# Kernel tuning notes

Hardware: AMD Instinct MI355X
Metric: run time of the kernel (lower is better)

## Reference

```python
import jax, jax.numpy as jnp
import numpy as np

B, K, N, M = 32, 128, 128, 256  # batch, num_classes(==n_dim), n_dim, samples-per-matrix
EPSILON = 0.1
LAMBDA_SOFTMAX = 0.1
LEARNING_RATE = 0.01
BN_EPS = 1e-5


def setup_inputs() -> dict:
    key = jax.random.key(0)
    k1, k2, k3 = jax.random.split(key, 3)
    x = jax.random.normal(k1, (B, N, M), dtype=jnp.float32)
    A = jax.random.normal(k2, (K, N, N), dtype=jnp.float32) * 0.1
    EC_proto = jnp.einsum('kij,klj->kil', A, A)  # per-class PSD prototype covariances (K,N,N)
    EC_count = jax.random.uniform(k3, (K,), dtype=jnp.float32, minval=1.0, maxval=100.0)
    return {"x": x, "EC_proto": EC_proto, "EC_count": EC_count}


def reference(x, EC_proto, EC_count):
    n = x.shape[1]
    dtype = x.dtype
    # BatchNorm1d(num_classes, affine=False, track_running_stats=False): batch stats over (N, L)
    mean = x.mean(axis=(0, 2), keepdims=True)
    var = x.var(axis=(0, 2), keepdims=True)  # biased variance, as torch uses for normalization
    x = (x - mean) / jnp.sqrt(var + BN_EPS)

    eye = jnp.eye(n, dtype=dtype)
    total = EC_count.sum()
    has_counts = total > 1e-6

    # E branch: global expansion operator
    e_alpha = jnp.where(has_counts, n / (EPSILON * EPSILON * total), jnp.zeros((), dtype))
    e = e_alpha * jnp.linalg.inv(e_alpha * EC_proto.sum(0) + eye)  # (N,N)
    e_x_z = jnp.einsum('ij,bjm->bim', e, x)  # (B,N,M)

    # C branch: per-class compression operators
    bool_depth = (EC_count != 0).astype(dtype)  # (K,)
    count_fix = EC_count + (1.0 - bool_depth)
    c_alpha = (n / (count_fix * EPSILON * EPSILON) * bool_depth)[:, None, None]  # (K,1,1)
    c = c_alpha * jnp.linalg.inv(c_alpha * EC_proto + eye[None])  # (K,N,N)
    c_x_z = jnp.einsum('kij,bjm->bkim', c, x)  # (B,K,N,M)

    # Frobenius norm per (b,k), rescaled to sum to 10 over classes
    norm = jnp.sqrt((c_x_z * c_x_z).sum(axis=(2, 3)))  # (B,K)
    norm = 10.0 * norm / norm.sum(axis=1, keepdims=True)

    pi = jax.nn.softmax(-LAMBDA_SOFTMAX * norm, axis=1) * bool_depth  # (B,K)
    gama = jnp.where(has_counts, EC_count / total, jnp.zeros_like(EC_count))  # (K,)

    z_d = e_x_z - jnp.einsum('k,bkim,bk->bim', gama, c_x_z, pi)  # (B,N,M)
    return x + LEARNING_RATE * z_d
```

## Files before the change

### kernel.cpp

```cpp
#include <hip/hip_runtime.h>
#include <math.h>

#define Bb 32
#define Kk 128
#define Nn 128
#define Mm 256
#define EPS2 0.01f
#define LAMBDA_S 0.1f
#define LR 0.01f
#define BN_EPS_C 1e-5f

#define SWZ(c) (((c) & 14) | (((c) & 1) << 4) | (((c) >> 4) & 1))

__device__ __forceinline__ float readlane_f(float v, int lane) {
  return __int_as_float(__builtin_amdgcn_readlane(__float_as_int(v), lane));
}

__global__ void kA_bn_psum(const float* __restrict__ x, const float* __restrict__ P,
                           float* __restrict__ xn, float* __restrict__ Psum) {
  int t = threadIdx.x;
  if (blockIdx.x < 128) {
    int n = blockIdx.x;
    float v[32];
    float s = 0.f, s2 = 0.f;
    #pragma unroll
    for (int b = 0; b < Bb; ++b) {
      v[b] = x[(size_t)b * (Nn * Mm) + n * Mm + t];
      s += v[b];
      s2 += v[b] * v[b];
    }
    #pragma unroll
    for (int o = 32; o > 0; o >>= 1) {
      s += __shfl_down(s, o, 64);
      s2 += __shfl_down(s2, o, 64);
    }
    __shared__ float rs[4], rs2[4];
    if ((t & 63) == 0) { rs[t >> 6] = s; rs2[t >> 6] = s2; }
    __syncthreads();
    float S = rs[0] + rs[1] + rs[2] + rs[3];
    float S2 = rs2[0] + rs2[1] + rs2[2] + rs2[3];
    float mean = S * (1.0f / (Bb * Mm));
    float var = S2 * (1.0f / (Bb * Mm)) - mean * mean;
    float rstd = 1.0f / sqrtf(var + BN_EPS_C);
    #pragma unroll
    for (int b = 0; b < Bb; ++b)
      xn[(size_t)b * (Nn * Mm) + n * Mm + t] = (v[b] - mean) * rstd;
  } else {
    int e = (blockIdx.x - 128) * 256 + t;
    float s = 0.f;
    #pragma unroll 8
    for (int k = 0; k < Kk; ++k) s += P[(size_t)k * 16384 + e];
    Psum[e] = s;
  }
}

__global__ __launch_bounds__(512, 1) void k3S(
    const float* __restrict__ P, const float* __restrict__ Psum,
    const float* __restrict__ cnt, float* __restrict__ C,
    const float* __restrict__ xn, float* __restrict__ S) {
  __shared__ __align__(16) float LB[8448];
  int bx = blockIdx.x;
  int t = threadIdx.x;

  if (bx < 129) {
    float* Mt = LB;
    float* Rb = LB + 2112;
    float* redc = LB + 4160;
    int mat = bx;
    int tx = t & 15;
    int wy = t >> 4;

    float cv = cnt[t & 127];
    float sr = cv;
    #pragma unroll
    for (int o = 32; o > 0; o >>= 1) sr += __shfl_down(sr, o, 64);
    if ((t & 63) == 0) redc[t >> 6] = sr;
    __syncthreads();
    float total = redc[0] + redc[1];
    bool has = total > 1e-6f;
    float av;
    if (mat < 128) {
      float c = cnt[mat];
      float bk = (c != 0.0f) ? 1.0f : 0.0f;
      float cfix = c + (1.0f - bk);
      av = (float)Nn / (cfix * EPS2) * bk;
    } else {
      av = has ? ((float)Nn / (EPS2 * total)) : 0.0f;
    }
    const float* src = (mat < 128) ? (P + (size_t)mat * 16384) : Psum;

    float a[4][8];
    #pragma unroll
    for (int i = 0; i < 4; ++i) {
      int row = wy * 4 + i;
      float4 p0 = *(const float4*)&src[row * 128 + tx * 8];
      float4 p1 = *(const float4*)&src[row * 128 + tx * 8 + 4];
      a[i][0] = av * p0.x; a[i][1] = av * p0.y; a[i][2] = av * p0.z; a[i][3] = av * p0.w;
      a[i][4] = av * p1.x; a[i][5] = av * p1.y; a[i][6] = av * p1.z; a[i][7] = av * p1.w;
      if (tx == (wy >> 1)) a[i][(wy & 1) * 4 + i] += 1.0f;
    }

    for (int kb = 0; kb < 8; ++kb) {
      int k0 = kb * 16;
      if ((wy >> 2) == kb) {
        int d = wy & 3;
        #pragma unroll
        for (int i = 0; i < 4; ++i) {
          *(float4*)&Rb[(d * 4 + i) * 128 + SWZ(2 * tx) * 4] =
              make_float4(a[i][0], a[i][1], a[i][2], a[i][3]);
          *(float4*)&Rb[(d * 4 + i) * 128 + SWZ(2 * tx + 1) * 4] =
              make_float4(a[i][4], a[i][5], a[i][6], a[i][7]);
        }
      }
      if ((tx >> 1) == kb) {
        int dh = tx & 1;
        #pragma unroll
        for (int i = 0; i < 4; ++i)
          #pragma unroll
          for (int j = 0; j < 8; ++j)
            Mt[(dh * 8 + j) * 132 + wy * 4 + i] = a[i][j];
      }
      __syncthreads();

      if (t < 64) {
        int l = t;
        float m[2][16];
        #pragma unroll
        for (int d = 0; d < 2; ++d)
          #pragma unroll
          for (int j = 0; j < 16; ++j)
            m[d][j] = Mt[j * 132 + 2 * l + d];
        #pragma unroll
        for (int q = 0; q < 16; ++q) {
          int lq = (k0 + q) >> 1;
          float pr[16];
          #pragma unroll
          for (int j = 0; j < 16; ++j) pr[j] = readlane_f(m[q & 1][j], lq);
          float piv = pr[q];
          float r0 = __builtin_amdgcn_rcpf(piv);
          float pinv = r0 * (2.0f - piv * r0);
          #pragma unroll
          for (int d = 0; d < 2; ++d) {
            float f = m[d][q];
            bool isp = (2 * l + d == k0 + q);
            float g = isp ? (1.0f - pinv) : f * pinv;
            #pragma unroll
            for (int j = 0; j < 16; ++j) m[d][j] = fmaf(-g, pr[j], m[d][j]);
            m[d][q] = isp ? pinv : -g;
          }
        }
        #pragma unroll
        for (int d = 0; d < 2; ++d)
          #pragma unroll
          for (int j = 0; j < 16; ++j)
            Mt[j * 132 + 2 * l + d] = m[d][j];
      }
      __syncthreads();

      if ((wy >> 2) == kb) {
        #pragma unroll
        for (int i = 0; i < 4; ++i)
          #pragma unroll
          for (int j = 0; j < 8; ++j) a[i][j] = 0.0f;
      }
      #pragma unroll
      for (int q = 0; q < 16; ++q) {
        float4 m0 = *(const float4*)&Mt[q * 132 + wy * 4];
        float4 r0 = *(const float4*)&Rb[q * 128 + SWZ(2 * tx) * 4];
        float4 r1 = *(const float4*)&Rb[q * 128 + SWZ(2 * tx + 1) * 4];
        float mq[4] = {m0.x, m0.y, m0.z, m0.w};
        float rq[8] = {r0.x, r0.y, r0.z, r0.w, r1.x, r1.y, r1.z, r1.w};
        #pragma unroll
        for (int i = 0; i < 4; ++i)
          #pragma unroll
          for (int j = 0; j < 8; ++j)
            a[i][j] = fmaf(mq[i], rq[j], a[i][j]);
      }
      if ((tx >> 1) == kb) {
        int dh = tx & 1;
        #pragma unroll
        for (int j = 0; j < 8; ++j) {
          float4 v0 = *(const float4*)&Mt[(dh * 8 + j) * 132 + wy * 4];
          a[0][j] = v0.x; a[1][j] = v0.y; a[2][j] = v0.z; a[3][j] = v0.w;
        }
      }
      __syncthreads();
    }

    float* dst = C + (size_t)mat * 16384;
    #pragma unroll
    for (int i = 0; i < 4; ++i) {
      int row = wy * 4 + i;
      float4 v0 = make_float4(av * a[i][0], av * a[i][1], av * a[i][2], av * a[i][3]);
      float4 v1 = make_float4(av * a[i][4], av * a[i][5], av * a[i][6], av * a[i][7]);
      *(float4*)&dst[row * 128 + tx * 8] = v0;
      *(float4*)&dst[row * 128 + tx * 8 + 4] = v1;
    }
  } else {
    int bxx = bx - 129;
    int b = bxx >> 1;
    int jbase = (bxx & 1) * 64;
    float* X = LB;
    int tx = t & 15, wy = t >> 4;
    float acc[4][4] = {};
    for (int mc = 0; mc < Mm; mc += 64) {
      __syncthreads();
      #pragma unroll
      for (int c = 0; c < 16; ++c) {
        int e = c * 512 + t;
        int i = e >> 6, mm = e & 63;
        X[i * 65 + mm] = xn[(size_t)b * (Nn * Mm) + i * Mm + mc + mm];
      }
      __syncthreads();
      for (int mm = 0; mm < 64; ++mm) {
        float ai[4], bj[4];
        #pragma unroll
        for (int q = 0; q < 4; ++q) ai[q] = X[(wy * 4 + q) * 65 + mm];
        #pragma unroll
        for (int q = 0; q < 4; ++q) bj[q] = X[(jbase + tx * 4 + q) * 65 + mm];
        #pragma unroll
        for (int qi = 0; qi < 4; ++qi)
          #pragma unroll
          for (int qj = 0; qj < 4; ++qj)
            acc[qi][qj] = fmaf(ai[qi], bj[qj], acc[qi][qj]);
      }
    }
    float* dst = S + (size_t)b * 16384;
    #pragma unroll
    for (int qi = 0; qi < 4; ++qi) {
      float4 v = make_float4(acc[qi][0], acc[qi][1], acc[qi][2], acc[qi][3]);
      *(float4*)&dst[(wy * 4 + qi) * 128 + jbase + tx * 4] = v;
    }
  }
}

__global__ __launch_bounds__(512, 1) void kGN(const float* __restrict__ C,
                                              const float* __restrict__ S,
                                              float* __restrict__ norm2h) {
  __shared__ __align__(16) float LB[128 * 128];
  __shared__ float redb[8][32];
  int k = blockIdx.x >> 1, h = blockIdx.x & 1;
  int t = threadIdx.x;
  const float* src = C + (size_t)k * 16384;
  #pragma unroll
  for (int c = 0; c < 32; ++c) LB[c * 512 + t] = src[c * 512 + t];
  __syncthreads();
  int tx = t & 15, ty = t >> 4;
  int i0 = ty * 4, j0 = h * 64 + tx * 4;
  float acc[4][4] = {};
  for (int l = 0; l < 128; ++l) {
    float ai[4], bj[4];
    *(float4*)&ai[0] = *(const float4*)&LB[l * 128 + i0];
    *(float4*)&bj[0] = *(const float4*)&LB[l * 128 + j0];
    #pragma unroll
    for (int qi = 0; qi < 4; ++qi)
      #pragma unroll
      for (int qj = 0; qj < 4; ++qj)
        acc[qi][qj] = fmaf(ai[qi], bj[qj], acc[qi][qj]);
  }
  float nacc[32];
  #pragma unroll
  for (int b = 0; b < 32; ++b) nacc[b] = 0.0f;
  #pragma unroll
  for (int qi = 0; qi < 4; ++qi) {
    const float* sb = S + (i0 + qi) * 128 + j0;
    #pragma unroll
    for (int b = 0; b < 32; ++b) {
      float4 sv = *(const float4*)&sb[(size_t)b * 16384];
      nacc[b] = fmaf(acc[qi][0], sv.x, nacc[b]);
      nacc[b] = fmaf(acc[qi][1], sv.y, nacc[b]);
      nacc[b] = fmaf(acc[qi][2], sv.z, nacc[b]);
      nacc[b] = fmaf(acc[qi][3], sv.w, nacc[b]);
    }
  }
  #pragma unroll
  for (int b = 0; b < 32; ++b) {
    float v = nacc[b];
    #pragma unroll
    for (int o = 32; o > 0; o >>= 1) v += __shfl_down(v, o, 64);
    nacc[b] = v;
  }
  if ((t & 63) == 0) {
    int w = t >> 6;
    #pragma unroll
    for (int b = 0; b < 32; ++b) redb[w][b] = nacc[b];
  }
  __syncthreads();
  if (t < 32) {
    float s = 0.f;
    #pragma unroll
    for (int w = 0; w < 8; ++w) s += redb[w][t];
    norm2h[(size_t)k * 64 + h * 32 + t] = s;
  }
}

__global__ __launch_bounds__(256, 1) void k8f(const float* __restrict__ C,
                                              const float* __restrict__ E,
                                              const float* __restrict__ norm2h,
                                              const float* __restrict__ cnt,
                                              float* __restrict__ F) {
  int t = threadIdx.x;
  int e = blockIdx.x * 256 + t;
  int b0 = blockIdx.y * 8;
  __shared__ float wTl[128][8];
  __shared__ float redT[2];
  __shared__ float redN[2][8];
  __shared__ float redE[2][8];

  float nb[8];
  float cv = 0.f;
  if (t < 128) {
    int k = t;
    cv = cnt[k];
    #pragma unroll
    for (int j = 0; j < 8; ++j) {
      float n2 = norm2h[(size_t)k * 64 + b0 + j] +
                 norm2h[(size_t)k * 64 + 32 + b0 + j];
      nb[j] = sqrtf(fmaxf(n2, 0.0f));
    }
    float tt = cv;
    float sn[8];
    #pragma unroll
    for (int j = 0; j < 8; ++j) sn[j] = nb[j];
    #pragma unroll
    for (int o = 32; o > 0; o >>= 1) {
      tt += __shfl_down(tt, o, 64);
      #pragma unroll
      for (int j = 0; j < 8; ++j) sn[j] += __shfl_down(sn[j], o, 64);
    }
    if ((t & 63) == 0) {
      redT[t >> 6] = tt;
      #pragma unroll
      for (int j = 0; j < 8; ++j) redN[t >> 6][j] = sn[j];
    }
  }
  __syncthreads();
  float exj[8];
  if (t < 128) {
    #pragma unroll
    for (int j = 0; j < 8; ++j) {
      float sumn = fmaxf(redN[0][j] + redN[1][j], 1e-30f);
      float nr = 10.0f * nb[j] / sumn;
      exj[j] = expf(-LAMBDA_S * nr);
    }
    float se[8];
    #pragma unroll
    for (int j = 0; j < 8; ++j) se[j] = exj[j];
    #pragma unroll
    for (int o = 32; o > 0; o >>= 1) {
      #pragma unroll
      for (int j = 0; j < 8; ++j) se[j] += __shfl_down(se[j], o, 64);
    }
    if ((t & 63) == 0) {
      #pragma unroll
      for (int j = 0; j < 8; ++j) redE[t >> 6][j] = se[j];
    }
  }
  __syncthreads();
  if (t < 128) {
    float total = redT[0] + redT[1];
    float bk = (cv != 0.0f) ? 1.0f : 0.0f;
    float gama = (total > 1e-6f) ? (cv / total) : 0.0f;
    #pragma unroll
    for (int j = 0; j < 8; ++j) {
      float sume = redE[0][j] + redE[1][j];
      float pi = (exj[j] / sume) * bk;
      wTl[t][j] = gama * pi;
    }
  }
  __syncthreads();

  float acc[8];
  float ev = E[e];
  #pragma unroll
  for (int b = 0; b < 8; ++b) acc[b] = ev;
  for (int k = 0; k < 128; ++k) {
    float cval = C[(size_t)k * 16384 + e];
    #pragma unroll
    for (int b = 0; b < 8; ++b) acc[b] = fmaf(-wTl[k][b], cval, acc[b]);
  }
  #pragma unroll
  for (int b = 0; b < 8; ++b) F[(size_t)(b0 + b) * 16384 + e] = acc[b];
}

__global__ __launch_bounds__(256, 1) void k9_k(const float* __restrict__ F,
                                               const float* __restrict__ xn,
                                               float* __restrict__ out) {
  int bx = blockIdx.x;
  int b = bx >> 3, y = bx & 7;
  int mq = y >> 1, ih = y & 1;
  __shared__ __align__(16) float Ft[64 * 68];
  __shared__ __align__(16) float Xt[64 * 68];
  int t = threadIdx.x;
  int tx = t & 15, ty = t >> 4;
  float acc[4][4] = {};
  for (int jc = 0; jc < 128; jc += 64) {
    __syncthreads();
    #pragma unroll
    for (int q = 0; q < 4; ++q) {
      int e = q * 256 + t;
      int i = e >> 4, j4 = e & 15;
      *(float4*)&Ft[i * 68 + j4 * 4] =
          *(const float4*)&F[(size_t)b * 16384 + (ih * 64 + i) * 128 + jc + j4 * 4];
    }
    #pragma unroll
    for (int q = 0; q < 4; ++q) {
      int e = q * 256 + t;
      int jj = e >> 4, m4 = e & 15;
      *(float4*)&Xt[jj * 68 + m4 * 4] =
          *(const float4*)&xn[(size_t)b * (Nn * Mm) + (jc + jj) * Mm + mq * 64 + m4 * 4];
    }
    __syncthreads();
    for (int j4 = 0; j4 < 16; ++j4) {
      float4 fi[4], xm[4];
      #pragma unroll
      for (int r = 0; r < 4; ++r)
        fi[r] = *(const float4*)&Ft[(ty * 4 + r) * 68 + j4 * 4];
      #pragma unroll
      for (int r = 0; r < 4; ++r)
        xm[r] = *(const float4*)&Xt[(j4 * 4 + r) * 68 + tx * 4];
      #pragma unroll
      for (int qi = 0; qi < 4; ++qi) {
        #pragma unroll
        for (int qm = 0; qm < 4; ++qm) {
          float xv = ((const float*)&xm[0])[qm];
          acc[qi][qm] = fmaf(fi[qi].x, xv, acc[qi][qm]);
          xv = ((const float*)&xm[1])[qm];
          acc[qi][qm] = fmaf(fi[qi].y, xv, acc[qi][qm]);
          xv = ((const float*)&xm[2])[qm];
          acc[qi][qm] = fmaf(fi[qi].z, xv, acc[qi][qm]);
          xv = ((const float*)&xm[3])[qm];
          acc[qi][qm] = fmaf(fi[qi].w, xv, acc[qi][qm]);
        }
      }
    }
  }
  int i0 = ih * 64 + ty * 4, m0 = mq * 64 + tx * 4;
  #pragma unroll
  for (int qi = 0; qi < 4; ++qi) {
    float4 xv = *(const float4*)&xn[(size_t)b * (Nn * Mm) + (i0 + qi) * Mm + m0];
    float4 o;
    o.x = fmaf(LR, acc[qi][0], xv.x);
    o.y = fmaf(LR, acc[qi][1], xv.y);
    o.z = fmaf(LR, acc[qi][2], xv.z);
    o.w = fmaf(LR, acc[qi][3], xv.w);
    *(float4*)&out[(size_t)b * (Nn * Mm) + (i0 + qi) * Mm + m0] = o;
  }
}

extern "C" void kernel_launch(void* const* d_in, const int* in_sizes, int n_in,
                              void* d_out, int out_size, void* d_ws, size_t ws_size,
                              hipStream_t stream) {
  const float* x = (const float*)d_in[0];
  const float* P = (const float*)d_in[1];
  const float* cnt = (const float*)d_in[2];
  float* out = (float*)d_out;

  float* ws = (float*)d_ws;
  float* xn = ws;
  float* C = xn + 1048576;
  float* S = C + 2113536;
  float* norm2h = S + 524288;
  float* F = norm2h + 8192;
  float* Psum = F + 524288;
  size_t need_bytes = (size_t)((Psum + 16384) - ws) * sizeof(float);
  if (ws_size < need_bytes) return;

  hipLaunchKernelGGL(kA_bn_psum, dim3(192), dim3(256), 0, stream, x, P, xn, Psum);
  hipLaunchKernelGGL(k3S, dim3(193), dim3(512), 0, stream, P, Psum, cnt, C, xn, S);
  hipLaunchKernelGGL(kGN, dim3(256), dim3(512), 0, stream, C, S, norm2h);
  hipLaunchKernelGGL(k8f, dim3(64, 4), dim3(256), 0, stream, C,
                     C + (size_t)128 * 16384, norm2h, cnt, F);
  hipLaunchKernelGGL(k9_k, dim3(256), dim3(256), 0, stream, F, xn, out);
}
```

Baseline: 163.4 us.

## Split kGN into quarter-column blocks and widen k9 blocks to 512 threads

Result: faster. 159.0 us (median of 2 runs) (-2.7%).

```diff
diff --git a/kernel.cpp b/kernel.cpp
--- a/kernel.cpp
+++ b/kernel.cpp
@@ -234,43 +234,52 @@
   }
 }
 
-__global__ __launch_bounds__(512, 1) void kGN(const float* __restrict__ C,
+__global__ __launch_bounds__(256, 1) void kGN(const float* __restrict__ C,
                                               const float* __restrict__ S,
                                               float* __restrict__ norm2h) {
   __shared__ __align__(16) float LB[128 * 128];
-  __shared__ float redb[8][32];
-  int k = blockIdx.x >> 1, h = blockIdx.x & 1;
+  __shared__ float redb[4][32];
+  int k = blockIdx.x >> 2, qh = blockIdx.x & 3;
   int t = threadIdx.x;
   const float* src = C + (size_t)k * 16384;
-  #pragma unroll
-  for (int c = 0; c < 32; ++c) LB[c * 512 + t] = src[c * 512 + t];
+  for (int c = 0; c < 64; ++c) LB[c * 256 + t] = src[c * 256 + t];
   __syncthreads();
   int tx = t & 15, ty = t >> 4;
-  int i0 = ty * 4, j0 = h * 64 + tx * 4;
-  float acc[4][4] = {};
+  int i0 = ty * 8, j0 = qh * 32 + tx * 2;
+  float acc[8][2] = {};
+  #pragma unroll 2
   for (int l = 0; l < 128; ++l) {
-    float ai[4], bj[4];
+    float ai[8];
     *(float4*)&ai[0] = *(const float4*)&LB[l * 128 + i0];
-    *(float4*)&bj[0] = *(const float4*)&LB[l * 128 + j0];
-    #pragma unroll
-    for (int qi = 0; qi < 4; ++qi)
-      #pragma unroll
-      for (int qj = 0; qj < 4; ++qj)
-        acc[qi][qj] = fmaf(ai[qi], bj[qj], acc[qi][qj]);
-  }
+    *(float4*)&ai[4] = *(const float4*)&LB[l * 128 + i0 + 4];
+    float2 bj = *(const float2*)&LB[l * 128 + j0];
+    #pragma unroll
+    for (int qi = 0; qi < 8; ++qi) {
+      acc[qi][0] = fmaf(ai[qi], bj.x, acc[qi][0]);
+      acc[qi][1] = fmaf(ai[qi], bj.y, acc[qi][1]);
+    }
+  }
+  __syncthreads();
+  #pragma unroll
+  for (int qi = 0; qi < 8; ++qi)
+    *(float2*)&LB[(i0 + qi) * 32 + tx * 2] = make_float2(acc[qi][0], acc[qi][1]);
+  __syncthreads();
   float nacc[32];
   #pragma unroll
   for (int b = 0; b < 32; ++b) nacc[b] = 0.0f;
   #pragma unroll
-  for (int qi = 0; qi < 4; ++qi) {
-    const float* sb = S + (i0 + qi) * 128 + j0;
+  for (int q = 0; q < 4; ++q) {
+    int el = (q * 256 + t) * 4;
+    float4 g = *(const float4*)&LB[el];
+    int i = el >> 5, jl = el & 31;
+    const float* sb = S + i * 128 + qh * 32 + jl;
     #pragma unroll
     for (int b = 0; b < 32; ++b) {
       float4 sv = *(const float4*)&sb[(size_t)b * 16384];
-      nacc[b] = fmaf(acc[qi][0], sv.x, nacc[b]);
-      nacc[b] = fmaf(acc[qi][1], sv.y, nacc[b]);
-      nacc[b] = fmaf(acc[qi][2], sv.z, nacc[b]);
-      nacc[b] = fmaf(acc[qi][3], sv.w, nacc[b]);
+      nacc[b] = fmaf(g.x, sv.x, nacc[b]);
+      nacc[b] = fmaf(g.y, sv.y, nacc[b]);
+      nacc[b] = fmaf(g.z, sv.z, nacc[b]);
+      nacc[b] = fmaf(g.w, sv.w, nacc[b]);
     }
   }
   #pragma unroll
@@ -286,12 +295,9 @@
     for (int b = 0; b < 32; ++b) redb[w][b] = nacc[b];
   }
   __syncthreads();
-  if (t < 32) {
-    float s = 0.f;
-    #pragma unroll
-    for (int w = 0; w < 8; ++w) s += redb[w][t];
-    norm2h[(size_t)k * 64 + h * 32 + t] = s;
-  }
+  if (t < 32)
+    norm2h[(size_t)k * 128 + qh * 32 + t] =
+        redb[0][t] + redb[1][t] + redb[2][t] + redb[3][t];
 }
 
 __global__ __launch_bounds__(256, 1) void k8f(const float* __restrict__ C,
@@ -314,8 +320,8 @@
     cv = cnt[k];
     #pragma unroll
     for (int j = 0; j < 8; ++j) {
-      float n2 = norm2h[(size_t)k * 64 + b0 + j] +
-                 norm2h[(size_t)k * 64 + 32 + b0 + j];
+      const float* nh = norm2h + (size_t)k * 128 + b0 + j;
+      float n2 = nh[0] + nh[32] + nh[64] + nh[96];
       nb[j] = sqrtf(fmaxf(n2, 0.0f));
     }
     float tt = cv;
@@ -374,6 +380,7 @@
   float ev = E[e];
   #pragma unroll
   for (int b = 0; b < 8; ++b) acc[b] = ev;
+  #pragma unroll 4
   for (int k = 0; k < 128; ++k) {
     float cval = C[(size_t)k * 16384 + e];
     #pragma unroll
@@ -383,7 +390,7 @@
   for (int b = 0; b < 8; ++b) F[(size_t)(b0 + b) * 16384 + e] = acc[b];
 }
 
-__global__ __launch_bounds__(256, 1) void k9_k(const float* __restrict__ F,
+__global__ __launch_bounds__(512, 1) void k9_k(const float* __restrict__ F,
                                                const float* __restrict__ xn,
                                                float* __restrict__ out) {
   int bx = blockIdx.x;
@@ -393,34 +400,34 @@
   __shared__ __align__(16) float Xt[64 * 68];
   int t = threadIdx.x;
   int tx = t & 15, ty = t >> 4;
-  float acc[4][4] = {};
+  float acc[2][4] = {};
   for (int jc = 0; jc < 128; jc += 64) {
     __syncthreads();
     #pragma unroll
-    for (int q = 0; q < 4; ++q) {
-      int e = q * 256 + t;
+    for (int q = 0; q < 2; ++q) {
+      int e = q * 512 + t;
       int i = e >> 4, j4 = e & 15;
       *(float4*)&Ft[i * 68 + j4 * 4] =
           *(const float4*)&F[(size_t)b * 16384 + (ih * 64 + i) * 128 + jc + j4 * 4];
     }
     #pragma unroll
-    for (int q = 0; q < 4; ++q) {
-      int e = q * 256 + t;
+    for (int q = 0; q < 2; ++q) {
+      int e = q * 512 + t;
       int jj = e >> 4, m4 = e & 15;
       *(float4*)&Xt[jj * 68 + m4 * 4] =
           *(const float4*)&xn[(size_t)b * (Nn * Mm) + (jc + jj) * Mm + mq * 64 + m4 * 4];
     }
     __syncthreads();
     for (int j4 = 0; j4 < 16; ++j4) {
-      float4 fi[4], xm[4];
-      #pragma unroll
-      for (int r = 0; r < 4; ++r)
-        fi[r] = *(const float4*)&Ft[(ty * 4 + r) * 68 + j4 * 4];
+      float4 fi[2], xm[4];
+      #pragma unroll
+      for (int r = 0; r < 2; ++r)
+        fi[r] = *(const float4*)&Ft[(ty * 2 + r) * 68 + j4 * 4];
       #pragma unroll
       for (int r = 0; r < 4; ++r)
         xm[r] = *(const float4*)&Xt[(j4 * 4 + r) * 68 + tx * 4];
       #pragma unroll
-      for (int qi = 0; qi < 4; ++qi) {
+      for (int qi = 0; qi < 2; ++qi) {
         #pragma unroll
         for (int qm = 0; qm < 4; ++qm) {
           float xv = ((const float*)&xm[0])[qm];
@@ -435,9 +442,9 @@
       }
     }
   }
-  int i0 = ih * 64 + ty * 4, m0 = mq * 64 + tx * 4;
-  #pragma unroll
-  for (int qi = 0; qi < 4; ++qi) {
+  int i0 = ih * 64 + ty * 2, m0 = mq * 64 + tx * 4;
+  #pragma unroll
+  for (int qi = 0; qi < 2; ++qi) {
     float4 xv = *(const float4*)&xn[(size_t)b * (Nn * Mm) + (i0 + qi) * Mm + m0];
     float4 o;
     o.x = fmaf(LR, acc[qi][0], xv.x);
@@ -461,15 +468,15 @@
   float* C = xn + 1048576;
   float* S = C + 2113536;
   float* norm2h = S + 524288;
-  float* F = norm2h + 8192;
+  float* F = norm2h + 16384;
   float* Psum = F + 524288;
   size_t need_bytes = (size_t)((Psum + 16384) - ws) * sizeof(float);
   if (ws_size < need_bytes) return;
 
   hipLaunchKernelGGL(kA_bn_psum, dim3(192), dim3(256), 0, stream, x, P, xn, Psum);
   hipLaunchKernelGGL(k3S, dim3(193), dim3(512), 0, stream, P, Psum, cnt, C, xn, S);
-  hipLaunchKernelGGL(kGN, dim3(256), dim3(512), 0, stream, C, S, norm2h);
+  hipLaunchKernelGGL(kGN, dim3(512), dim3(256), 0, stream, C, S, norm2h);
   hipLaunchKernelGGL(k8f, dim3(64, 4), dim3(256), 0, stream, C,
                      C + (size_t)128 * 16384, norm2h, cnt, F);
-  hipLaunchKernelGGL(k9_k, dim3(256), dim3(256), 0, stream, F, xn, out);
-}
+  hipLaunchKernelGGL(k9_k, dim3(256), dim3(512), 0, stream, F, xn, out);
+}
```
